# Kernel optimization log

Measured on AMD Instinct MI355X. Metric: run time of the kernel, lower is better.

## Reference

```python
import jax, jax.numpy as jnp
import numpy as np

B, A, C = 128, 8732, 21

def setup_inputs() -> dict:
    key = jax.random.key(0)
    k1, k2, k3, k4 = jax.random.split(key, 4)
    return {
        "location_output": jax.random.normal(k1, (B, A, 4), dtype=jnp.float32),
        "classifi_output": jax.random.normal(k2, (B, A, C), dtype=jnp.float32),
        "location_label": jax.random.normal(k3, (B, A, 4), dtype=jnp.float32),
        "classifi_label": jax.random.randint(k4, (B, A), 0, C, dtype=jnp.int64),
    }

def reference(location_output, classifi_output, location_label, classifi_label):
    mask = classifi_label > 0                      # [B, A] positive anchors
    pos_num = mask.sum(axis=1)                     # [B]

    # SmoothL1 (beta=1), summed over the 4 box coords, masked to positives
    diff = location_output - location_label
    ad = jnp.abs(diff)
    sl1 = jnp.where(ad < 1.0, 0.5 * diff * diff, ad - 0.5).sum(axis=-1)  # [B, A]
    loc_loss = (sl1 * mask.astype(sl1.dtype)).sum(axis=-1)               # [B]

    # Per-anchor cross entropy
    logp = jax.nn.log_softmax(classifi_output, axis=-1)                  # [B, A, C]
    con = -jnp.take_along_axis(logp, classifi_label[..., None], axis=-1)[..., 0]  # [B, A]

    # Hard negative mining: rank negatives by CE (descending), keep top 3*pos_num
    con_neg = jnp.where(mask, 0.0, con)
    rank = jnp.argsort(jnp.argsort(-con_neg, axis=1), axis=1)            # rank in descending order
    neg_num = jnp.minimum(3 * pos_num, A)
    neg_num = jnp.where(neg_num == 0, 3, neg_num)
    neg_mask = rank < neg_num[:, None]

    con_loss = (con * (mask.astype(con.dtype) + neg_mask.astype(con.dtype))).sum(axis=1)  # [B]

    total = loc_loss + con_loss
    denom = jnp.where(pos_num != 0, pos_num, 1).astype(total.dtype)
    return (total / denom).mean()
```

## Files before the change

kernel.cpp:

```cpp
#include <hip/hip_runtime.h>

#define NBATCH 128
#define NANCH  8732
#define NCLS   21
#define SUBS   8
#define SUBLEN 1092
#define ROUNDS 5


__device__ __forceinline__ float waveReduceF(float v) {
    #pragma unroll
    for (int o = 32; o > 0; o >>= 1) v += __shfl_down(v, o, 64);
    return v;
}
__device__ __forceinline__ unsigned waveReduceU(unsigned v) {
    #pragma unroll
    for (int o = 32; o > 0; o >>= 1) v += __shfl_down(v, o, 64);
    return v;
}

__device__ __forceinline__ float con_from_row(const float* __restrict__ row, int lbl) {
    float m = row[0];
    #pragma unroll
    for (int c = 1; c < NCLS; ++c) m = fmaxf(m, row[c]);
    float s = 0.f;
    #pragma unroll
    for (int c = 0; c < NCLS; ++c) s += __expf(row[c] - m);
    return m + __logf(s) - row[lbl];
}

__device__ __forceinline__ void gload_lds16(const float4* g, float4* l) {
    __builtin_amdgcn_global_load_lds(
        (const __attribute__((address_space(1))) void*)g,
        (__attribute__((address_space(3))) void*)l,
        16, 0, 0);
}

__global__ __launch_bounds__(256) void anchor_kernel(
    const float*  __restrict__ loc_out,
    const float*  __restrict__ cls_out,
    const float*  __restrict__ loc_lab,
    const int*    __restrict__ labels,
    float4* __restrict__ partial)
{
    __shared__ float ldsrow[256 * NCLS];

    const int bid  = blockIdx.x;
    const int b    = bid >> 3;
    const int sub  = bid & 7;
    const int tid  = threadIdx.x;
    const int start = sub * SUBLEN;
    const int len   = (sub == 7) ? (NANCH - 7 * SUBLEN) : SUBLEN;
    const int wbase = (tid >> 6) << 6;

    float loc_s = 0.f, all_s = 0.f, pos_s = 0.f;
    unsigned pc = 0;

    for (int r = 0; r < ROUNDS; ++r) {
        const int al    = r * 256 + tid;
        const bool valid = al < len;
        const int nA    = min(256, len - r * 256);
        const int nF4   = (nA * NCLS) >> 2;

        const size_t rbase = ((size_t)b * NANCH + start + r * 256) * NCLS;
        const float4* gsrc = reinterpret_cast<const float4*>(cls_out + rbase);

        int lbl = 0; float4 lo4 = {}; float4 ll4 = {};
        if (valid) {
            const size_t ba = (size_t)b * NANCH + start + al;
            lbl = labels[ba];
            lo4 = ((const float4*)loc_out)[ba];
            ll4 = ((const float4*)loc_lab)[ba];
        }

        if (r) __syncthreads();
        float4* lbase = (float4*)ldsrow;
        #pragma unroll
        for (int i = 0; i < 6; ++i) {
            const int idx = i * 256 + tid;
            if (idx < nF4)
                gload_lds16(gsrc + idx, lbase + i * 256 + wbase);
        }
        __syncthreads();

        if (valid) {
            const float* __restrict__ row = ldsrow + tid * NCLS;
            float f[NCLS];
            #pragma unroll
            for (int c = 0; c < NCLS; ++c) f[c] = row[c];

            float m = f[0];
            #pragma unroll
            for (int c = 1; c < NCLS; ++c) m = fmaxf(m, f[c]);
            float s = 0.f;
            #pragma unroll
            for (int c = 0; c < NCLS; ++c) s += __expf(f[c] - m);

            const float tgt = row[lbl];
            const float con = m + __logf(s) - tgt;
            all_s += con;
            if (lbl > 0) {
                pos_s += con;
                pc++;
                float d0 = lo4.x - ll4.x, d1 = lo4.y - ll4.y,
                      d2 = lo4.z - ll4.z, d3 = lo4.w - ll4.w;
                float a0 = fabsf(d0), a1 = fabsf(d1), a2 = fabsf(d2), a3 = fabsf(d3);
                loc_s += ((a0 < 1.f) ? 0.5f * d0 * d0 : (a0 - 0.5f))
                       + ((a1 < 1.f) ? 0.5f * d1 * d1 : (a1 - 0.5f))
                       + ((a2 < 1.f) ? 0.5f * d2 * d2 : (a2 - 0.5f))
                       + ((a3 < 1.f) ? 0.5f * d3 * d3 : (a3 - 0.5f));
            }
        }
    }

    loc_s = waveReduceF(loc_s);
    all_s = waveReduceF(all_s);
    pos_s = waveReduceF(pos_s);
    pc    = waveReduceU(pc);

    __shared__ float sL[4], sA[4], sP[4];
    __shared__ unsigned sC[4];
    const int w = tid >> 6, lane = tid & 63;
    if (lane == 0) { sL[w] = loc_s; sA[w] = all_s; sP[w] = pos_s; sC[w] = pc; }
    __syncthreads();
    if (tid == 0) {
        float L = sL[0] + sL[1] + sL[2] + sL[3];
        float S = sA[0] + sA[1] + sA[2] + sA[3];
        float P = sP[0] + sP[1] + sP[2] + sP[3];
        unsigned C = sC[0] + sC[1] + sC[2] + sC[3];
        partial[bid] = make_float4(L, S, P, (float)C);
    }
}

__global__ __launch_bounds__(256) void finalize_kernel(
    const float* __restrict__ cls_out,
    const int*   __restrict__ labels,
    const float4* __restrict__ partial,
    float* __restrict__ out)
{
    const int tid = threadIdx.x;

    __shared__ float sLoc[NBATCH], sPos[NBATCH], sCnt[NBATCH], sConl[NBATCH];
    __shared__ unsigned sK[NBATCH];
    __shared__ unsigned nflag;
    if (tid == 0) nflag = 0;
    __syncthreads();

    if (tid < NBATCH) {
        float loc = 0.f, all = 0.f, pos = 0.f, cnt = 0.f;
        #pragma unroll
        for (int c = 0; c < SUBS; ++c) {
            float4 p = partial[tid * SUBS + c];
            loc += p.x; all += p.y; pos += p.z; cnt += p.w;
        }
        unsigned k = 3u * (unsigned)cnt;
        if (k > NANCH) k = NANCH;
        if (k == 0u) k = 3u;
        sLoc[tid] = loc; sPos[tid] = pos; sCnt[tid] = cnt;
        sConl[tid] = all + pos;
        if (k < NANCH) { sK[tid] = k; atomicAdd(&nflag, 1u); }
        else sK[tid] = 0u;
    }
    __syncthreads();

    if (nflag) {
        __shared__ float    rF[256];
        __shared__ unsigned rU[256];
        for (int b2 = 0; b2 < NBATCH; ++b2) {
            unsigned k = sK[b2];
            if (!k) continue;

            auto count_gt = [&](float t) -> unsigned {
                unsigned cc = 0;
                for (int an = tid; an < NANCH; an += 256) {
                    size_t ba = (size_t)b2 * NANCH + an;
                    int lbl = labels[ba];
                    if (lbl > 0) continue;
                    float con = con_from_row(cls_out + ba * NCLS, lbl);
                    if (con > t) cc++;
                }
                rU[tid] = cc; __syncthreads();
                for (int o = 128; o > 0; o >>= 1) {
                    if (tid < o) rU[tid] += rU[tid + o];
                    __syncthreads();
                }
                unsigned r = rU[0]; __syncthreads();
                return r;
            };

            unsigned cpos = count_gt(0.0f);
            float negpart = 0.f;

            if (k <= cpos) {
                unsigned lo = 0u, hi = 0x7F800000u;
                while (hi - lo > 1u) {
                    unsigned mid = lo + (hi - lo) / 2u;
                    unsigned cc = count_gt(__uint_as_float(mid));
                    if (cc >= k) lo = mid; else hi = mid;
                }
                float v = __uint_as_float(hi);
                float ss = 0.f; unsigned c1 = 0;
                for (int an = tid; an < NANCH; an += 256) {
                    size_t ba = (size_t)b2 * NANCH + an;
                    int lbl = labels[ba];
                    if (lbl > 0) continue;
                    float con = con_from_row(cls_out + ba * NCLS, lbl);
                    if (con > v) { ss += con; c1++; }
                }
                rF[tid] = ss; rU[tid] = c1; __syncthreads();
                for (int o = 128; o > 0; o >>= 1) {
                    if (tid < o) { rF[tid] += rF[tid + o]; rU[tid] += rU[tid + o]; }
                    __syncthreads();
                }
                negpart = rF[0] + (float)(k - rU[0]) * v;
                __syncthreads();
            } else {
                if (tid == 0) {
                    float np = 0.f;
                    unsigned mrem = k - cpos;
                    for (int an = 0; an < NANCH; ++an) {
                        size_t ba = (size_t)b2 * NANCH + an;
                        int lbl = labels[ba];
                        float con = con_from_row(cls_out + ba * NCLS, lbl);
                        float cneg = (lbl > 0) ? 0.f : con;
                        if (cneg > 0.f) np += con;
                        else if (mrem > 0u) { np += con; mrem--; }
                    }
                    rF[0] = np;
                }
                __syncthreads();
                negpart = rF[0];
                __syncthreads();
            }

            if (tid == 0) sConl[b2] = sPos[b2] + negpart;
            __syncthreads();
        }
    }

    float t = 0.f;
    if (tid < NBATCH) {
        float denom = (sCnt[tid] != 0.f) ? sCnt[tid] : 1.f;
        t = (sLoc[tid] + sConl[tid]) / denom;
    }
    t = waveReduceF(t);
    __shared__ float sW[4];
    const int w = tid >> 6, lane = tid & 63;
    if (lane == 0) sW[w] = t;
    __syncthreads();
    if (tid == 0) out[0] = (sW[0] + sW[1] + sW[2] + sW[3]) * (1.f / NBATCH);
}

extern "C" void kernel_launch(void* const* d_in, const int* in_sizes, int n_in,
                              void* d_out, int out_size, void* d_ws, size_t ws_size,
                              hipStream_t stream) {
    const float* loc_out = (const float*)d_in[0];
    const float* cls_out = (const float*)d_in[1];
    const float* loc_lab = (const float*)d_in[2];
    const int*   labels  = (const int*)d_in[3];
    float* out = (float*)d_out;
    float4* partial = (float4*)d_ws;

    anchor_kernel<<<NBATCH * SUBS, 256, 0, stream>>>(loc_out, cls_out, loc_lab, labels, partial);
    finalize_kernel<<<1, 256, 0, stream>>>(cls_out, labels, partial, out);
}
```

Measured before the change: 176.5 us.

## Replace LDS-staged rounds with direct per-thread vector loads of four anchors

The anchor kernel no longer stages class logits through LDS with async global-to-LDS copies and barriers over several rounds. Each thread now handles four consecutive anchors, loading their 84 logits as 21 float4s straight into registers, together with labels as an int4 and the box data. The grid becomes 2D, 9 x 128 single-round blocks, with a launch-bounds occupancy hint. This removes the LDS traffic and the synchronisation, at the cost of strided, less coalesced per-lane global loads and higher register pressure from the 84-element array.

```diff
diff --git a/kernel.cpp b/kernel.cpp
--- a/kernel.cpp
+++ b/kernel.cpp
@@ -3,9 +3,8 @@
 #define NBATCH 128
 #define NANCH  8732
 #define NCLS   21
-#define SUBS   8
-#define SUBLEN 1092
-#define ROUNDS 5
+#define GRPS   2183
+#define SUBS   9
 
 
 __device__ __forceinline__ float waveReduceF(float v) {
@@ -29,82 +28,65 @@
     return m + __logf(s) - row[lbl];
 }
 
-__device__ __forceinline__ void gload_lds16(const float4* g, float4* l) {
-    __builtin_amdgcn_global_load_lds(
-        (const __attribute__((address_space(1))) void*)g,
-        (__attribute__((address_space(3))) void*)l,
-        16, 0, 0);
-}
-
-__global__ __launch_bounds__(256) void anchor_kernel(
+__global__ __launch_bounds__(256, 3) void anchor_kernel(
     const float*  __restrict__ loc_out,
     const float*  __restrict__ cls_out,
     const float*  __restrict__ loc_lab,
     const int*    __restrict__ labels,
     float4* __restrict__ partial)
 {
-    __shared__ float ldsrow[256 * NCLS];
-
-    const int bid  = blockIdx.x;
-    const int b    = bid >> 3;
-    const int sub  = bid & 7;
-    const int tid  = threadIdx.x;
-    const int start = sub * SUBLEN;
-    const int len   = (sub == 7) ? (NANCH - 7 * SUBLEN) : SUBLEN;
-    const int wbase = (tid >> 6) << 6;
+    const int b   = blockIdx.y;
+    const int s   = blockIdx.x;
+    const int tid = threadIdx.x;
+    const int g   = s * 256 + tid;
 
     float loc_s = 0.f, all_s = 0.f, pos_s = 0.f;
     unsigned pc = 0;
 
-    for (int r = 0; r < ROUNDS; ++r) {
-        const int al    = r * 256 + tid;
-        const bool valid = al < len;
-        const int nA    = min(256, len - r * 256);
-        const int nF4   = (nA * NCLS) >> 2;
-
-        const size_t rbase = ((size_t)b * NANCH + start + r * 256) * NCLS;
-        const float4* gsrc = reinterpret_cast<const float4*>(cls_out + rbase);
-
-        int lbl = 0; float4 lo4 = {}; float4 ll4 = {};
-        if (valid) {
-            const size_t ba = (size_t)b * NANCH + start + al;
-            lbl = labels[ba];
-            lo4 = ((const float4*)loc_out)[ba];
-            ll4 = ((const float4*)loc_lab)[ba];
-        }
-
-        if (r) __syncthreads();
-        float4* lbase = (float4*)ldsrow;
-        #pragma unroll
-        for (int i = 0; i < 6; ++i) {
-            const int idx = i * 256 + tid;
-            if (idx < nF4)
-                gload_lds16(gsrc + idx, lbase + i * 256 + wbase);
-        }
-        __syncthreads();
-
-        if (valid) {
-            const float* __restrict__ row = ldsrow + tid * NCLS;
-            float f[NCLS];
+    if (g < GRPS) {
+        const size_t ba0 = (size_t)b * NANCH + (size_t)g * 4;
+
+        const int4 lbl4 = *(const int4*)(labels + ba0);
+        const float4* __restrict__ cp = (const float4*)(cls_out + ba0 * NCLS);
+        float f[84];
+        #pragma unroll
+        for (int i = 0; i < 21; ++i) {
+            const float4 v = cp[i];
+            f[4*i+0] = v.x; f[4*i+1] = v.y; f[4*i+2] = v.z; f[4*i+3] = v.w;
+        }
+        float4 lo[4], ll[4];
+        #pragma unroll
+        for (int j = 0; j < 4; ++j) {
+            lo[j] = ((const float4*)loc_out)[ba0 + j];
+            ll[j] = ((const float4*)loc_lab)[ba0 + j];
+        }
+        int lbls[4] = { lbl4.x, lbl4.y, lbl4.z, lbl4.w };
+
+        #pragma unroll
+        for (int j = 0; j < 4; ++j) {
+            const int lbl = lbls[j];
+            float m   = f[21*j];
+            float tgt = f[21*j];
             #pragma unroll
-            for (int c = 0; c < NCLS; ++c) f[c] = row[c];
-
-            float m = f[0];
+            for (int cc = 1; cc < NCLS; ++cc) {
+                const float v = f[21*j + cc];
+                m = fmaxf(m, v);
+                tgt = (cc == lbl) ? v : tgt;
+            }
+            float sum = 0.f;
             #pragma unroll
-            for (int c = 1; c < NCLS; ++c) m = fmaxf(m, f[c]);
-            float s = 0.f;
-            #pragma unroll
-            for (int c = 0; c < NCLS; ++c) s += __expf(f[c] - m);
-
-            const float tgt = row[lbl];
-            const float con = m + __logf(s) - tgt;
+            for (int cc = 0; cc < NCLS; ++cc)
+                sum += __expf(f[21*j + cc] - m);
+
+            const float con = m + __logf(sum) - tgt;
             all_s += con;
             if (lbl > 0) {
                 pos_s += con;
                 pc++;
-                float d0 = lo4.x - ll4.x, d1 = lo4.y - ll4.y,
-                      d2 = lo4.z - ll4.z, d3 = lo4.w - ll4.w;
-                float a0 = fabsf(d0), a1 = fabsf(d1), a2 = fabsf(d2), a3 = fabsf(d3);
+                const float d0 = lo[j].x - ll[j].x, d1 = lo[j].y - ll[j].y,
+                            d2 = lo[j].z - ll[j].z, d3 = lo[j].w - ll[j].w;
+                const float a0 = fabsf(d0), a1 = fabsf(d1),
+                            a2 = fabsf(d2), a3 = fabsf(d3);
                 loc_s += ((a0 < 1.f) ? 0.5f * d0 * d0 : (a0 - 0.5f))
                        + ((a1 < 1.f) ? 0.5f * d1 * d1 : (a1 - 0.5f))
                        + ((a2 < 1.f) ? 0.5f * d2 * d2 : (a2 - 0.5f))
@@ -128,7 +110,7 @@
         float S = sA[0] + sA[1] + sA[2] + sA[3];
         float P = sP[0] + sP[1] + sP[2] + sP[3];
         unsigned C = sC[0] + sC[1] + sC[2] + sC[3];
-        partial[bid] = make_float4(L, S, P, (float)C);
+        partial[b * SUBS + s] = make_float4(L, S, P, (float)C);
     }
 }
 
@@ -261,6 +243,7 @@
     float* out = (float*)d_out;
     float4* partial = (float4*)d_ws;
 
-    anchor_kernel<<<NBATCH * SUBS, 256, 0, stream>>>(loc_out, cls_out, loc_lab, labels, partial);
+    dim3 grid(SUBS, NBATCH);
+    anchor_kernel<<<grid, 256, 0, stream>>>(loc_out, cls_out, loc_lab, labels, partial);
     finalize_kernel<<<1, 256, 0, stream>>>(cls_out, labels, partial, out);
 }
```

Result: no change. 177.8 us (+0.8%).
